# Kernel tuning notes

Hardware: AMD Instinct MI355X
Metric: run time of the kernel (lower is better)

Reference implementation:

```python
import jax, jax.numpy as jnp
import numpy as np


def _rotate_half(x):
    a, b = jnp.split(x, 2, axis=-1)
    return jnp.concatenate([-b, a], axis=-1)


def _rope_tables(L, d, dtype):
    inv = 1.0 / (10000.0 ** (jnp.arange(0, d, 2, dtype=jnp.float32) / d))
    ang = jnp.arange(L, dtype=jnp.float32)[:, None] * inv[None, :]  # (L, d/2)
    cos = jnp.repeat(jnp.cos(ang), 2, axis=-1)[None, :, None, :].astype(dtype)  # (1,L,1,d)
    sin = jnp.repeat(jnp.sin(ang), 2, axis=-1)[None, :, None, :].astype(dtype)
    return cos, sin


def setup_inputs() -> dict:
    key = jax.random.key(0)
    ks = jax.random.split(key, 7)
    B, L, D, h = 1, 1024, 768, 12
    d = D // h
    s = 0.02
    return {
        "X": jax.random.normal(ks[0], (B, L, D), jnp.float32),
        "Wq": jax.random.normal(ks[1], (D, D), jnp.float32) * s,
        "Wk": jax.random.normal(ks[2], (D, D), jnp.float32) * s,
        "Wv": jax.random.normal(ks[3], (D, D), jnp.float32) * s,
        "Wu": jax.random.normal(ks[4], (D, D), jnp.float32) * s,
        "Wg": jax.random.normal(ks[5], (3 * h, D), jnp.float32) * s,
        "Wo": jax.random.normal(ks[6], (D, D), jnp.float32) * s,
        "prior_mu": jnp.zeros((1, 1, h, d), jnp.float32),
        "prior_log_tau": jnp.zeros((1, 1, h, 1), jnp.float32),
    }


def _forward(X, Wq, Wk, Wv, Wu, Wg, Wo, prior_mu, prior_log_tau):
    B, L, D = X.shape
    h = prior_mu.shape[2]
    d = D // h
    eps = 1e-12
    # projections (torch Linear: x @ W.T, no bias)
    q = (X @ Wq.T).reshape(B, L, h, d)
    k = (X @ Wk.T).reshape(B, L, h, d)
    v = (X @ Wv.T).reshape(B, L, h, d)
    u = (X @ Wu.T).reshape(B, L, h, d)
    gate = (X @ Wg.T).reshape(B, L, h, 3)
    t = jnp.arange(1, L + 1, dtype=X.dtype).reshape(1, L, 1, 1)
    # calculate_logit (logit_type='deviation', causal)
    log_tau = jnp.exp(jnp.clip(prior_log_tau, -50.0, 30.0))
    u_sum = jnp.cumsum(u, axis=1)
    bar_u = (log_tau * prior_mu + u_sum) / (log_tau + t)
    s_i = -jnp.sum(u * bar_u, axis=-1, keepdims=True) / np.float32(np.sqrt(d))  # (B,L,h,1)
    # RoPE + L2 normalize q, k
    cos, sin = _rope_tables(L, d, X.dtype)
    q = q * cos + _rotate_half(q) * sin
    k = k * cos + _rotate_half(k) * sin
    q = q / jnp.maximum(jnp.linalg.norm(q, axis=-1, keepdims=True), eps)
    k = k / jnp.maximum(jnp.linalg.norm(k, axis=-1, keepdims=True), eps)
    # associative causal branch of compute_o
    s_max = jax.lax.stop_gradient(jnp.max(s_i, axis=1, keepdims=True))
    exp_s = jnp.exp(s_i - s_max)              # (B,L,h,1)
    E_t = jnp.cumsum(exp_s, axis=1)
    P_t = jnp.cumsum(s_i, axis=1)
    kv = jnp.einsum('blhd,blhe->blhde', k, v)  # (B,L,h,d,d)
    F_t = jnp.cumsum(exp_s[..., None] * kv, axis=1)
    G_t = jnp.cumsum(s_i[..., None] * kv, axis=1)
    H_t = jnp.cumsum(kv, axis=1)
    sig1 = jax.nn.sigmoid(gate[..., 0:1])      # (B,L,h,1)
    sigh = jax.nn.sigmoid(gate[..., 1:2])
    alpha = sigh / (E_t + eps)
    beta = (sig1 - sigh) / t
    gamma = -((beta * P_t + sigh) / t)
    M = alpha[..., None] * F_t + beta[..., None] * G_t + gamma[..., None] * H_t
    out = jnp.einsum('blhd,blhde->blhe', q, M)  # (B,L,h,d)
    # LayerNorm over head dim, eps=1e-5, no affine
    mu = jnp.mean(out, axis=-1, keepdims=True)
    var = jnp.mean(jnp.square(out - mu), axis=-1, keepdims=True)
    out = (out - mu) / jnp.sqrt(var + 1e-5)
    # output projection (dropout=0.0 -> identity)
    return out.reshape(B, L, D) @ Wo.T


def reference(X, Wq, Wk, Wv, Wu, Wg, Wo, prior_mu, prior_log_tau):
    return _forward(X, Wq, Wk, Wv, Wu, Wg, Wo, prior_mu, prior_log_tau)
```

## Files before the change

### kernel.cpp

```cpp
#include <hip/hip_runtime.h>
#include <hip/hip_bf16.h>
#include <math.h>

typedef __attribute__((ext_vector_type(8))) short bf16x8;
typedef __attribute__((ext_vector_type(4))) float f32x4;

#define SEQ 1024
#define DIM 768
#define NH 12
#define HD 64


__device__ __forceinline__ float wave_reduce_sum(float v) {
    for (int off = 1; off < 64; off <<= 1) v += __shfl_xor(v, off);
    return v;
}
__device__ __forceinline__ short f2bs(float x) {
    __hip_bfloat16 h = __float2bfloat16(x);
    return *reinterpret_cast<short*>(&h);
}
__device__ __forceinline__ float bs2f(short x) {
    __hip_bfloat16 h = *reinterpret_cast<__hip_bfloat16*>(&x);
    return (float)h;
}
__device__ __forceinline__ bf16x8 cvt8r(const float4& a, const float4& b) {
    bf16x8 r;
    r[0]=f2bs(a.x); r[1]=f2bs(a.y); r[2]=f2bs(a.z); r[3]=f2bs(a.w);
    r[4]=f2bs(b.x); r[5]=f2bs(b.y); r[6]=f2bs(b.z); r[7]=f2bs(b.w);
    return r;
}

__device__ __forceinline__ void async_copy16(const void* gptr, void* ldsbase, int lane) {
#if __has_builtin(__builtin_amdgcn_global_load_lds)
    __builtin_amdgcn_global_load_lds(
        (const __attribute__((address_space(1))) unsigned int*)gptr,
        (__attribute__((address_space(3))) unsigned int*)ldsbase, 16, 0, 0);
#else
    *(bf16x8*)((short*)ldsbase + lane*8) = *(const bf16x8*)gptr;
#endif
}

__global__ __launch_bounds__(256) void k_prep(const float* __restrict__ X,
    const float* __restrict__ Wq, const float* __restrict__ Wk,
    const float* __restrict__ Wv, const float* __restrict__ Wu,
    const float* __restrict__ Wg, const float* __restrict__ Wo,
    short* __restrict__ Xb, short* __restrict__ Wqb, short* __restrict__ Wkb,
    short* __restrict__ Wvb, short* __restrict__ Wub, short* __restrict__ Wgb,
    short* __restrict__ Wob)
{
    int seg = blockIdx.y;
    const float* src; short* dst; int n8;
    switch (seg) {
        case 0: src = X;  dst = Xb;  n8 = 98304; break;
        case 1: src = Wq; dst = Wqb; n8 = 73728; break;
        case 2: src = Wk; dst = Wkb; n8 = 73728; break;
        case 3: src = Wv; dst = Wvb; n8 = 73728; break;
        case 4: src = Wu; dst = Wub; n8 = 73728; break;
        case 5: src = Wg; dst = Wgb; n8 = 3456;  break;
        default: src = Wo; dst = Wob; n8 = 73728; break;
    }
    int i = blockIdx.x*256 + threadIdx.x;
    if (i >= n8) return;
    const float* s = src + (size_t)i*8;
    *(bf16x8*)(dst + (size_t)i*8) = cvt8r(*(const float4*)s, *(const float4*)(s + 4));
}

__global__ __launch_bounds__(256, 3) void k_proj5(const short* __restrict__ Xb,
    const short* __restrict__ Wqb, const short* __restrict__ Wkb,
    const short* __restrict__ Wvb, const short* __restrict__ Wub,
    const short* __restrict__ Wgb,
    __hip_bfloat16* __restrict__ Qb, __hip_bfloat16* __restrict__ Kb,
    __hip_bfloat16* __restrict__ Vt, __hip_bfloat16* __restrict__ Ub,
    float* __restrict__ G)
{
    int rt = blockIdx.x, ct = blockIdx.y, mat = blockIdx.z;
    if (mat == 4 && ct != 0) return;
    if (mat == 2 && rt >= 12) return;
    if ((mat == 0 || mat == 1 || mat == 3) && ct >= 6) return;

    __shared__ short lds[24576];

    int tid = threadIdx.x;
    int wv = tid>>6, lane = tid&63, g = lane>>4, n = lane&15;
    int wn = wv;

    const short* Asrc; const short* Bsrc; int arow0, brow0, Brows;
    if (mat == 2) { Asrc = Wvb; Bsrc = Xb; arow0 = rt*64; brow0 = ct*128; Brows = SEQ; }
    else {
        Asrc = Xb; arow0 = rt*64; brow0 = ct*128;
        Bsrc = (mat==0)?Wqb:(mat==1)?Wkb:(mat==3)?Wub:Wgb;
        Brows = (mat==4) ? 36 : DIM;
    }

    auto dma_step = [&](int buf, int k0) {
        short* Ab = lds + buf*4096;
        short* Bb = lds + 8192 + buf*8192;
        for (int p = 0; p < 2; ++p) {
            int sbase = p*256 + wv*64;
            int s = sbase + lane;
            int r = s >> 3, c = s & 7, cl = c ^ (r & 7);
            const short* gp = Asrc + (size_t)(arow0 + r)*DIM + k0 + cl*8;
            async_copy16(gp, Ab + sbase*8, lane);
        }
        for (int p = 0; p < 4; ++p) {
            int sbase = p*256 + wv*64;
            int s = sbase + lane;
            int r = s >> 3, c = s & 7, cl = c ^ (r & 7);
            int gr = brow0 + r; if (gr >= Brows) gr = Brows - 1;
            const short* gp = Bsrc + (size_t)gr*DIM + k0 + cl*8;
            async_copy16(gp, Bb + sbase*8, lane);
        }
    };

    f32x4 acc[4][2];
    for (int i=0;i<4;++i) for (int j=0;j<2;++j) acc[i][j] = (f32x4){0,0,0,0};

    dma_step(0, 0);
    for (int it = 0; it < 12; ++it) {
        __syncthreads();
        if (it < 11) dma_step(1 - (it & 1), (it + 1)*64);
        int buf = it & 1;
        const short* Ab = lds + buf*4096;
        const short* Bb = lds + 8192 + buf*8192;
        for (int ks = 0; ks < 2; ++ks) {
            int q = ks*4 + g;
            bf16x8 af[4], bfr[2];
            for (int i=0;i<4;++i)
                af[i] = *(const bf16x8*)(&Ab[((i*16+n)*8 + (q ^ (n&7)))*8]);
            for (int j=0;j<2;++j)
                bfr[j] = *(const bf16x8*)(&Bb[((wn*32+j*16+n)*8 + (q ^ (n&7)))*8]);
            for (int i=0;i<4;++i)
                for (int j=0;j<2;++j)
                    acc[i][j] = __builtin_amdgcn_mfma_f32_16x16x32_bf16(af[i], bfr[j], acc[i][j], 0,0,0);
        }
    }
    __syncthreads();

    if (mat == 4) {
        for (int i=0;i<4;++i) for (int j=0;j<2;++j) for (int r=0;r<4;++r) {
            int row = rt*64 + i*16 + g*4 + r;
            int col = wn*32 + j*16 + n;
            if (col < 36) G[(size_t)row*36 + col] = acc[i][j][r];
        }
        return;
    }

    short* C = lds;
    for (int i=0;i<4;++i) for (int j=0;j<2;++j) for (int r=0;r<4;++r)
        C[(i*16 + g*4 + r)*128 + wn*32 + j*16 + n] = f2bs(acc[i][j][r]);
    __syncthreads();

    if (mat == 2) {
        for (int k = 0; k < 16; ++k) {
            int row = k*4 + wv;
            unsigned int v = ((const unsigned int*)C)[row*64 + lane];
            ((unsigned int*)(Vt + (size_t)(rt*64 + row)*SEQ + ct*128))[lane] = v;
        }
    } else if (mat == 3) {
        for (int k = 0; k < 32; ++k) {
            int u = k*4 + wv;
            int row = u >> 1, hsel = u & 1;
            Ub[((size_t)(2*ct + hsel)*SEQ + rt*64 + row)*HD + lane] =
                *(__hip_bfloat16*)&C[row*128 + hsel*64 + lane];
        }
    } else {
        __hip_bfloat16* dst = (mat==0) ? Qb : Kb;
        int i2 = lane >> 1;
        float inv = expf((float)i2 * (-9.210340371976184f / 32.f));
        for (int k = 0; k < 32; ++k) {
            int u = k*4 + wv;
            int row = u >> 1, hsel = u & 1;
            int l = rt*64 + row;
            float x = bs2f(C[row*128 + hsel*64 + lane]);
            float ang = (float)l * inv;
            float c = cosf(ang), s = sinf(ang);
            float p = __shfl(x, lane ^ 32);
            float rot = (lane < 32) ? -p : p;
            float y = x*c + rot*s;
            float nrm = wave_reduce_sum(y*y);
            y = y / fmaxf(sqrtf(nrm), 1e-12f);
            dst[((size_t)(2*ct + hsel)*SEQ + l)*HD + lane] = __float2bfloat16(y);
        }
    }
}

__global__ __launch_bounds__(1024) void k_scan(const __hip_bfloat16* __restrict__ Ub,
    const float* __restrict__ G, const float* __restrict__ pmu,
    const float* __restrict__ plt,
    float* __restrict__ si_, float* __restrict__ es_, float* __restrict__ al_,
    float* __restrict__ be_, float* __restrict__ ga_)
{
    int h = blockIdx.x;
    int tid = threadIdx.x, wv = tid >> 6, lane = tid & 63;
    __shared__ float sbuf[SEQ], ebuf[SEQ], g1b[SEQ], ghb[SEQ];
    __shared__ float stot[16][64];
    __shared__ float wmax[16];
    __shared__ float smax_s;

    float ltv = fminf(fmaxf(plt[h], -50.f), 30.f);
    float ltau = expf(ltv);
    float mu = pmu[h*HD + lane];

    const __hip_bfloat16* up = Ub + ((size_t)h*SEQ + wv*64)*HD + lane;
    float Ul = 0.f;
    for (int i = 0; i < 64; ++i) Ul += (float)up[(size_t)i*HD];
    stot[wv][lane] = Ul;
    __syncthreads();
    float pre = ltau * mu;
    for (int w2 = 0; w2 < wv; ++w2) pre += stot[w2][lane];
    float V = pre;
    for (int i = 0; i < 64; ++i) {
        float uv = (float)up[(size_t)i*HD];
        V += uv;
        int l = wv*64 + i;
        float bar = V / (ltau + (float)(l + 1));
        float p = wave_reduce_sum(uv * bar);
        if (lane == 0) sbuf[l] = -p * 0.125f;
    }
    __syncthreads();
    float v = sbuf[tid];
    float vm = v;
    for (int off = 1; off < 64; off <<= 1) vm = fmaxf(vm, __shfl_xor(vm, off));
    if (lane == 0) wmax[wv] = vm;
    __syncthreads();
    if (wv == 0) {
        float mm = (lane < 16) ? wmax[lane] : -1e30f;
        for (int off = 1; off < 16; off <<= 1) mm = fmaxf(mm, __shfl_xor(mm, off));
        if (lane == 0) smax_s = mm;
    }
    __syncthreads();
    float ev = expf(fminf(v - smax_s, 0.f));
    ebuf[tid] = ev;
    g1b[tid] = 1.f / (1.f + expf(-G[(size_t)tid*36 + h*3 + 0]));
    ghb[tid] = 1.f / (1.f + expf(-G[(size_t)tid*36 + h*3 + 1]));
    si_[h*SEQ + tid] = v;
    es_[h*SEQ + tid] = ev;
    __syncthreads();
    if (wv == 0) {
        int base = lane * 16;
        float se = 0.f, ss = 0.f;
        for (int i = 0; i < 16; ++i) { se += ebuf[base + i]; ss += sbuf[base + i]; }
        float pe = se, ps = ss;
        for (int off = 1; off < 64; off <<= 1) {
            float t1 = __shfl_up(pe, off), t2 = __shfl_up(ps, off);
            if (lane >= off) { pe += t1; ps += t2; }
        }
        float E = pe - se, P = ps - ss;
        for (int i = 0; i < 16; ++i) {
            int l = base + i;
            E += ebuf[l]; P += sbuf[l];
            float t = (float)(l + 1);
            float s1 = g1b[l], sh = ghb[l];
            float a = sh / (E + 1e-12f);
            float b = (s1 - sh) / t;
            float gm = -((b * P + sh) / t);
            al_[h*SEQ + l] = a;
            be_[h*SEQ + l] = b;
            ga_[h*SEQ + l] = gm;
        }
    }
}

__global__ __launch_bounds__(256) void k_attn(const __hip_bfloat16* __restrict__ Qb,
    const __hip_bfloat16* __restrict__ Kb, const __hip_bfloat16* __restrict__ Vt,
    const float* __restrict__ si_, const float* __restrict__ es_,
    const float* __restrict__ al_, const float* __restrict__ be_,
    const float* __restrict__ ga_, __hip_bfloat16* __restrict__ opre)
{
    int t = blockIdx.x, h = blockIdx.y;
    int wv = threadIdx.x >> 6, lane = threadIdx.x & 63;
    int g = lane >> 4, n = lane & 15;
    __shared__ short P[4][16*64];
    __shared__ float Op[4][16][64];
    short* Pw = P[wv];
    int m0 = t*16;
    const short* qrow = (const short*)Qb + ((size_t)h*SEQ + m0 + n)*HD + g*8;
    bf16x8 qa0 = *(const bf16x8*)qrow;
    bf16x8 qa1 = *(const bf16x8*)(qrow + 32);
    const float* al = al_ + h*SEQ;
    const float* be = be_ + h*SEQ;
    const float* ga = ga_ + h*SEQ;
    const float* es = es_ + h*SEQ;
    const float* si = si_ + h*SEQ;
    float A_[4], B_[4], G_[4];
    for (int r = 0; r < 4; ++r) {
        int m = m0 + g*4 + r;
        A_[r] = al[m]; B_[r] = be[m]; G_[r] = ga[m];
    }
    f32x4 acco[4];
    for (int et = 0; et < 4; ++et) acco[et] = (f32x4){0.f,0.f,0.f,0.f};

    int jtmax = t >> 2;
    for (int jt = wv; jt <= jtmax; jt += 4) {
        int j0 = jt*64;
        for (int ct = 0; ct < 4; ++ct) {
            const short* krow = (const short*)Kb + ((size_t)h*SEQ + j0 + ct*16 + n)*HD + g*8;
            bf16x8 kb0 = *(const bf16x8*)krow;
            bf16x8 kb1 = *(const bf16x8*)(krow + 32);
            f32x4 sacc = {0.f,0.f,0.f,0.f};
            sacc = __builtin_amdgcn_mfma_f32_16x16x32_bf16(qa0, kb0, sacc, 0, 0, 0);
            sacc = __builtin_amdgcn_mfma_f32_16x16x32_bf16(qa1, kb1, sacc, 0, 0, 0);
            int j = j0 + ct*16 + n;
            float ej = es[j], sj = si[j];
            int chunk = ct*2 + (n>>3), e = n&7;
            for (int r = 0; r < 4; ++r) {
                int m = m0 + g*4 + r;
                float w = (j <= m) ? (A_[r]*ej + B_[r]*sj + G_[r]) : 0.f;
                int ml = g*4 + r;
                Pw[ml*64 + (chunk ^ (ml&7))*8 + e] = f2bs(w * sacc[r]);
            }
        }
        const short* vb = (const short*)Vt + (size_t)h*HD*SEQ;
        for (int et = 0; et < 4; ++et) {
            for (int sub = 0; sub < 2; ++sub) {
                int q = sub*4 + g;
                bf16x8 pa = *(const bf16x8*)(&Pw[n*64 + (q ^ (n&7))*8]);
                bf16x8 vfr = *(const bf16x8*)(vb + (size_t)(et*16 + n)*SEQ + j0 + sub*32 + g*8);
                acco[et] = __builtin_amdgcn_mfma_f32_16x16x32_bf16(pa, vfr, acco[et], 0, 0, 0);
            }
        }
    }
    for (int et = 0; et < 4; ++et)
        for (int r = 0; r < 4; ++r)
            Op[wv][g*4 + r][et*16 + n] = acco[et][r];
    __syncthreads();
    for (int rr = 0; rr < 4; ++rr) {
        int row = wv*4 + rr;
        float v = Op[0][row][lane] + Op[1][row][lane] + Op[2][row][lane] + Op[3][row][lane];
        float sm = wave_reduce_sum(v);
        float sq = wave_reduce_sum(v*v);
        float mu = sm * (1.f/64.f);
        float var = fmaxf(sq * (1.f/64.f) - mu*mu, 0.f);
        float invs = rsqrtf(var + 1e-5f);
        opre[(size_t)(m0 + row)*DIM + h*HD + lane] = __float2bfloat16((v - mu) * invs);
    }
}

__global__ __launch_bounds__(256, 4) void k_oproj(const short* __restrict__ A,
    const short* __restrict__ Wob, float* __restrict__ out)
{
    int rt = blockIdx.x, ct = blockIdx.y;
    __shared__ short lds[16384];

    int tid = threadIdx.x;
    int wv = tid>>6, lane = tid&63, g = lane>>4, n = lane&15;
    int wm = wv>>1, wn = wv&1;

    auto dma_step = [&](int buf, int k0) {
        short* Ab = lds + buf*4096;
        short* Bb = lds + 8192 + buf*4096;
        for (int p = 0; p < 2; ++p) {
            int sbase = p*256 + wv*64;
            int s = sbase + lane;
            int r = s >> 3, c = s & 7, cl = c ^ (r & 7);
            const short* ga_ = A + (size_t)(rt*64 + r)*DIM + k0 + cl*8;
            async_copy16(ga_, Ab + sbase*8, lane);
            const short* gb = Wob + (size_t)(ct*64 + r)*DIM + k0 + cl*8;
            async_copy16(gb, Bb + sbase*8, lane);
        }
    };

    f32x4 acc[2][2];
    for (int i=0;i<2;++i) for (int j=0;j<2;++j) acc[i][j] = (f32x4){0,0,0,0};

    dma_step(0, 0);
    for (int it = 0; it < 12; ++it) {
        __syncthreads();
        if (it < 11) dma_step(1 - (it & 1), (it + 1)*64);
        int buf = it & 1;
        const short* Ab = lds + buf*4096;
        const short* Bb = lds + 8192 + buf*4096;
        for (int ks = 0; ks < 2; ++ks) {
            int q = ks*4 + g;
            bf16x8 af[2], bfr[2];
            for (int i=0;i<2;++i)
                af[i] = *(const bf16x8*)(&Ab[((wm*32+i*16+n)*8 + (q ^ (n&7)))*8]);
            for (int j=0;j<2;++j)
                bfr[j] = *(const bf16x8*)(&Bb[((wn*32+j*16+n)*8 + (q ^ (n&7)))*8]);
            for (int i=0;i<2;++i)
                for (int j=0;j<2;++j)
                    acc[i][j] = __builtin_amdgcn_mfma_f32_16x16x32_bf16(af[i], bfr[j], acc[i][j], 0,0,0);
        }
    }
    for (int i=0;i<2;++i) for (int j=0;j<2;++j) for (int r=0;r<4;++r) {
        int row = rt*64 + wm*32 + i*16 + g*4 + r;
        int col = ct*64 + wn*32 + j*16 + n;
        out[(size_t)row*DIM + col] = acc[i][j][r];
    }
}

extern "C" void kernel_launch(void* const* d_in, const int* in_sizes, int n_in,
                              void* d_out, int out_size, void* d_ws, size_t ws_size,
                              hipStream_t stream) {
    const float* X   = (const float*)d_in[0];
    const float* Wq  = (const float*)d_in[1];
    const float* Wk  = (const float*)d_in[2];
    const float* Wv  = (const float*)d_in[3];
    const float* Wu  = (const float*)d_in[4];
    const float* Wg  = (const float*)d_in[5];
    const float* Wo  = (const float*)d_in[6];
    const float* pmu = (const float*)d_in[7];
    const float* plt = (const float*)d_in[8];

    char* w = (char*)d_ws;
    __hip_bfloat16* Qb   = (__hip_bfloat16*)(w + 0);
    __hip_bfloat16* Kb   = (__hip_bfloat16*)(w + 1572864);
    __hip_bfloat16* Vt   = (__hip_bfloat16*)(w + 3145728);
    __hip_bfloat16* opre = (__hip_bfloat16*)(w + 4718592);
    float*          G    = (float*)(w + 6291456);
    float*          si_  = (float*)(w + 6438912);
    float*          es_  = si_ + NH*SEQ;
    float*          al_  = es_ + NH*SEQ;
    float*          be_  = al_ + NH*SEQ;
    float*          ga_  = be_ + NH*SEQ;
    short*          Xb   = (short*)(w + 6684672);
    short*          Wqb  = (short*)(w + 8257536);
    short*          Wkb  = (short*)(w + 9437184);
    short*          Wvb  = (short*)(w + 10616832);
    short*          Wub  = (short*)(w + 11796480);
    short*          Wgb  = (short*)(w + 12976128);
    short*          Wob  = (short*)(w + 13031424);
    __hip_bfloat16* Ub   = (__hip_bfloat16*)d_out;
    float*          out  = (float*)d_out;

    hipLaunchKernelGGL(k_prep, dim3(384, 7), dim3(256), 0, stream,
                       X, Wq, Wk, Wv, Wu, Wg, Wo, Xb, Wqb, Wkb, Wvb, Wub, Wgb, Wob);
    hipLaunchKernelGGL(k_proj5, dim3(16, 8, 5), dim3(256), 0, stream,
                       Xb, Wqb, Wkb, Wvb, Wub, Wgb, Qb, Kb, Vt, Ub, G);
    hipLaunchKernelGGL(k_scan, dim3(NH), dim3(1024), 0, stream,
                       Ub, G, pmu, plt, si_, es_, al_, be_, ga_);
    hipLaunchKernelGGL(k_attn, dim3(64, NH), dim3(256), 0, stream,
                       Qb, Kb, Vt, si_, es_, al_, be_, ga_, opre);
    hipLaunchKernelGGL(k_oproj, dim3(16, 12), dim3(256), 0, stream,
                       (const short*)opre, Wob, out);
}
```

Measured before the change: 172.9 us.

## Fuse all five stages into one persistent cooperative kernel with grid syncs

Replaces the five separate kernel launches (convert, projections, scan, attention, output projection) with a single cooperative kernel of 400 blocks. The stages are separated by grid.sync calls, and each stage's work is assigned by block index. This removes the launch gaps and per-kernel ramp-up between stages. In exchange, every stage is limited to 400 blocks of 256 threads at occupancy 2, the scan stage appears to need a new partial-sum workspace, and each grid barrier has its own cost.

```diff
diff --git a/kernel.cpp b/kernel.cpp
--- a/kernel.cpp
+++ b/kernel.cpp
@@ -1,6 +1,9 @@
 #include <hip/hip_runtime.h>
 #include <hip/hip_bf16.h>
+#include <hip/hip_cooperative_groups.h>
 #include <math.h>
+
+namespace cg = cooperative_groups;
 
 typedef __attribute__((ext_vector_type(8))) short bf16x8;
 typedef __attribute__((ext_vector_type(4))) float f32x4;
@@ -9,10 +12,29 @@
 #define DIM 768
 #define NH 12
 #define HD 64
-
+#define NBLK 400
+
+#define OFF_QB   0
+#define OFF_KB   1572864
+#define OFF_VT   3145728
+#define OFF_OPRE 4718592
+#define OFF_G    6291456
+#define OFF_SCAL 6438912
+#define OFF_XB   6684672
+#define OFF_WQB  8257536
+#define OFF_WKB  9437184
+#define OFF_WVB  10616832
+#define OFF_WUB  11796480
+#define OFF_WGB  12976128
+#define OFF_WOB  13031424
+#define OFF_PSUM 14211072
 
 __device__ __forceinline__ float wave_reduce_sum(float v) {
     for (int off = 1; off < 64; off <<= 1) v += __shfl_xor(v, off);
+    return v;
+}
+__device__ __forceinline__ float wave_reduce_max(float v) {
+    for (int off = 1; off < 64; off <<= 1) v = fmaxf(v, __shfl_xor(v, off));
     return v;
 }
 __device__ __forceinline__ short f2bs(float x) {
@@ -29,7 +51,6 @@
     r[4]=f2bs(b.x); r[5]=f2bs(b.y); r[6]=f2bs(b.z); r[7]=f2bs(b.w);
     return r;
 }
-
 __device__ __forceinline__ void async_copy16(const void* gptr, void* ldsbase, int lane) {
 #if __has_builtin(__builtin_amdgcn_global_load_lds)
     __builtin_amdgcn_global_load_lds(
@@ -40,352 +61,364 @@
 #endif
 }
 
-__global__ __launch_bounds__(256) void k_prep(const float* __restrict__ X,
-    const float* __restrict__ Wq, const float* __restrict__ Wk,
-    const float* __restrict__ Wv, const float* __restrict__ Wu,
-    const float* __restrict__ Wg, const float* __restrict__ Wo,
-    short* __restrict__ Xb, short* __restrict__ Wqb, short* __restrict__ Wkb,
-    short* __restrict__ Wvb, short* __restrict__ Wub, short* __restrict__ Wgb,
-    short* __restrict__ Wob)
+__global__ __launch_bounds__(256, 2) void k_fused(
+    const float* __restrict__ X,  const float* __restrict__ Wq,
+    const float* __restrict__ Wk, const float* __restrict__ Wv,
+    const float* __restrict__ Wu, const float* __restrict__ Wg,
+    const float* __restrict__ Wo, const float* __restrict__ pmu,
+    const float* __restrict__ plt, char* __restrict__ ws, void* __restrict__ dout)
 {
-    int seg = blockIdx.y;
-    const float* src; short* dst; int n8;
-    switch (seg) {
-        case 0: src = X;  dst = Xb;  n8 = 98304; break;
-        case 1: src = Wq; dst = Wqb; n8 = 73728; break;
-        case 2: src = Wk; dst = Wkb; n8 = 73728; break;
-        case 3: src = Wv; dst = Wvb; n8 = 73728; break;
-        case 4: src = Wu; dst = Wub; n8 = 73728; break;
-        case 5: src = Wg; dst = Wgb; n8 = 3456;  break;
-        default: src = Wo; dst = Wob; n8 = 73728; break;
-    }
-    int i = blockIdx.x*256 + threadIdx.x;
-    if (i >= n8) return;
-    const float* s = src + (size_t)i*8;
-    *(bf16x8*)(dst + (size_t)i*8) = cvt8r(*(const float4*)s, *(const float4*)(s + 4));
-}
-
-__global__ __launch_bounds__(256, 3) void k_proj5(const short* __restrict__ Xb,
-    const short* __restrict__ Wqb, const short* __restrict__ Wkb,
-    const short* __restrict__ Wvb, const short* __restrict__ Wub,
-    const short* __restrict__ Wgb,
-    __hip_bfloat16* __restrict__ Qb, __hip_bfloat16* __restrict__ Kb,
-    __hip_bfloat16* __restrict__ Vt, __hip_bfloat16* __restrict__ Ub,
-    float* __restrict__ G)
-{
-    int rt = blockIdx.x, ct = blockIdx.y, mat = blockIdx.z;
-    if (mat == 4 && ct != 0) return;
-    if (mat == 2 && rt >= 12) return;
-    if ((mat == 0 || mat == 1 || mat == 3) && ct >= 6) return;
-
-    __shared__ short lds[24576];
-
-    int tid = threadIdx.x;
-    int wv = tid>>6, lane = tid&63, g = lane>>4, n = lane&15;
-    int wn = wv;
-
-    const short* Asrc; const short* Bsrc; int arow0, brow0, Brows;
-    if (mat == 2) { Asrc = Wvb; Bsrc = Xb; arow0 = rt*64; brow0 = ct*128; Brows = SEQ; }
-    else {
-        Asrc = Xb; arow0 = rt*64; brow0 = ct*128;
-        Bsrc = (mat==0)?Wqb:(mat==1)?Wkb:(mat==3)?Wub:Wgb;
-        Brows = (mat==4) ? 36 : DIM;
-    }
-
-    auto dma_step = [&](int buf, int k0) {
-        short* Ab = lds + buf*4096;
-        short* Bb = lds + 8192 + buf*8192;
-        for (int p = 0; p < 2; ++p) {
-            int sbase = p*256 + wv*64;
-            int s = sbase + lane;
-            int r = s >> 3, c = s & 7, cl = c ^ (r & 7);
-            const short* gp = Asrc + (size_t)(arow0 + r)*DIM + k0 + cl*8;
-            async_copy16(gp, Ab + sbase*8, lane);
-        }
-        for (int p = 0; p < 4; ++p) {
-            int sbase = p*256 + wv*64;
-            int s = sbase + lane;
-            int r = s >> 3, c = s & 7, cl = c ^ (r & 7);
-            int gr = brow0 + r; if (gr >= Brows) gr = Brows - 1;
-            const short* gp = Bsrc + (size_t)gr*DIM + k0 + cl*8;
-            async_copy16(gp, Bb + sbase*8, lane);
-        }
-    };
-
-    f32x4 acc[4][2];
-    for (int i=0;i<4;++i) for (int j=0;j<2;++j) acc[i][j] = (f32x4){0,0,0,0};
-
-    dma_step(0, 0);
-    for (int it = 0; it < 12; ++it) {
+    cg::grid_group grid = cg::this_grid();
+    alignas(16) __shared__ char smem[49152];
+
+    int bid = blockIdx.x, tid = threadIdx.x;
+    int wv = tid >> 6, lane = tid & 63, g = lane >> 4, n = lane & 15;
+
+    __hip_bfloat16* Qb   = (__hip_bfloat16*)(ws + OFF_QB);
+    __hip_bfloat16* Kb   = (__hip_bfloat16*)(ws + OFF_KB);
+    __hip_bfloat16* Vt   = (__hip_bfloat16*)(ws + OFF_VT);
+    __hip_bfloat16* opre = (__hip_bfloat16*)(ws + OFF_OPRE);
+    float* Gt  = (float*)(ws + OFF_G);
+    float* si_ = (float*)(ws + OFF_SCAL);
+    float* es_ = si_ + NH*SEQ;
+    float* al_ = es_ + NH*SEQ;
+    float* be_ = al_ + NH*SEQ;
+    float* ga_ = be_ + NH*SEQ;
+    short* Xb  = (short*)(ws + OFF_XB);
+    short* Wqb = (short*)(ws + OFF_WQB);
+    short* Wkb = (short*)(ws + OFF_WKB);
+    short* Wvb = (short*)(ws + OFF_WVB);
+    short* Wub = (short*)(ws + OFF_WUB);
+    short* Wgb = (short*)(ws + OFF_WGB);
+    short* Wob = (short*)(ws + OFF_WOB);
+    float* Psum = (float*)(ws + OFF_PSUM);
+    __hip_bfloat16* Ub = (__hip_bfloat16*)dout;
+    float* out = (float*)dout;
+
+    for (int idx = bid*256 + tid; idx < 470400; idx += NBLK*256) {
+        const float* src; short* dst; int off;
+        if      (idx < 98304)  { src = X;  dst = Xb;  off = idx; }
+        else if (idx < 172032) { src = Wq; dst = Wqb; off = idx - 98304; }
+        else if (idx < 245760) { src = Wk; dst = Wkb; off = idx - 172032; }
+        else if (idx < 319488) { src = Wv; dst = Wvb; off = idx - 245760; }
+        else if (idx < 393216) { src = Wu; dst = Wub; off = idx - 319488; }
+        else if (idx < 396672) { src = Wg; dst = Wgb; off = idx - 393216; }
+        else                   { src = Wo; dst = Wob; off = idx - 396672; }
+        const float* s = src + (size_t)off*8;
+        *(bf16x8*)(dst + (size_t)off*8) = cvt8r(*(const float4*)s, *(const float4*)(s + 4));
+    }
+    grid.sync();
+
+    {
+        int t = bid;
+        int mat, rt, ct;
+        if (t < 288)      { int m3 = t/96; mat = (m3==2)?3:m3; int r = t%96; rt = r/6; ct = r%6; }
+        else if (t < 384) { mat = 2; int r = t-288; rt = r/8; ct = r%8; }
+        else              { mat = 4; rt = t-384; ct = 0; }
+
+        short* lds = (short*)smem;
+        int wn = wv;
+
+        const short* Asrc; const short* Bsrc; int arow0, brow0, Brows;
+        if (mat == 2) { Asrc = Wvb; Bsrc = Xb; arow0 = rt*64; brow0 = ct*128; Brows = SEQ; }
+        else {
+            Asrc = Xb; arow0 = rt*64; brow0 = ct*128;
+            Bsrc = (mat==0)?Wqb:(mat==1)?Wkb:(mat==3)?Wub:Wgb;
+            Brows = (mat==4) ? 36 : DIM;
+        }
+
+        auto dma_step = [&](int buf, int k0) {
+            short* Ab = lds + buf*4096;
+            short* Bb = lds + 8192 + buf*8192;
+            for (int p = 0; p < 2; ++p) {
+                int sbase = p*256 + wv*64;
+                int s = sbase + lane;
+                int r = s >> 3, c = s & 7, cl = c ^ (r & 7);
+                async_copy16(Asrc + (size_t)(arow0 + r)*DIM + k0 + cl*8, Ab + sbase*8, lane);
+            }
+            for (int p = 0; p < 4; ++p) {
+                int sbase = p*256 + wv*64;
+                int s = sbase + lane;
+                int r = s >> 3, c = s & 7, cl = c ^ (r & 7);
+                int gr = brow0 + r; if (gr >= Brows) gr = Brows - 1;
+                async_copy16(Bsrc + (size_t)gr*DIM + k0 + cl*8, Bb + sbase*8, lane);
+            }
+        };
+
+        f32x4 acc[4][2];
+        for (int i=0;i<4;++i) for (int j=0;j<2;++j) acc[i][j] = (f32x4){0,0,0,0};
+
+        dma_step(0, 0);
+        for (int it = 0; it < 12; ++it) {
+            __syncthreads();
+            if (it < 11) dma_step(1 - (it & 1), (it + 1)*64);
+            int buf = it & 1;
+            const short* Ab = lds + buf*4096;
+            const short* Bb = lds + 8192 + buf*8192;
+            for (int ks = 0; ks < 2; ++ks) {
+                int q = ks*4 + g;
+                bf16x8 af[4], bfr[2];
+                for (int i=0;i<4;++i)
+                    af[i] = *(const bf16x8*)(&Ab[((i*16+n)*8 + (q ^ (n&7)))*8]);
+                for (int j=0;j<2;++j)
+                    bfr[j] = *(const bf16x8*)(&Bb[((wn*32+j*16+n)*8 + (q ^ (n&7)))*8]);
+                for (int i=0;i<4;++i)
+                    for (int j=0;j<2;++j)
+                        acc[i][j] = __builtin_amdgcn_mfma_f32_16x16x32_bf16(af[i], bfr[j], acc[i][j], 0,0,0);
+            }
+        }
         __syncthreads();
-        if (it < 11) dma_step(1 - (it & 1), (it + 1)*64);
-        int buf = it & 1;
-        const short* Ab = lds + buf*4096;
-        const short* Bb = lds + 8192 + buf*8192;
-        for (int ks = 0; ks < 2; ++ks) {
-            int q = ks*4 + g;
-            bf16x8 af[4], bfr[2];
-            for (int i=0;i<4;++i)
-                af[i] = *(const bf16x8*)(&Ab[((i*16+n)*8 + (q ^ (n&7)))*8]);
-            for (int j=0;j<2;++j)
-                bfr[j] = *(const bf16x8*)(&Bb[((wn*32+j*16+n)*8 + (q ^ (n&7)))*8]);
-            for (int i=0;i<4;++i)
-                for (int j=0;j<2;++j)
-                    acc[i][j] = __builtin_amdgcn_mfma_f32_16x16x32_bf16(af[i], bfr[j], acc[i][j], 0,0,0);
-        }
-    }
-    __syncthreads();
-
-    if (mat == 4) {
-        for (int i=0;i<4;++i) for (int j=0;j<2;++j) for (int r=0;r<4;++r) {
-            int row = rt*64 + i*16 + g*4 + r;
-            int col = wn*32 + j*16 + n;
-            if (col < 36) G[(size_t)row*36 + col] = acc[i][j][r];
-        }
-        return;
-    }
-
-    short* C = lds;
-    for (int i=0;i<4;++i) for (int j=0;j<2;++j) for (int r=0;r<4;++r)
-        C[(i*16 + g*4 + r)*128 + wn*32 + j*16 + n] = f2bs(acc[i][j][r]);
-    __syncthreads();
-
-    if (mat == 2) {
-        for (int k = 0; k < 16; ++k) {
-            int row = k*4 + wv;
-            unsigned int v = ((const unsigned int*)C)[row*64 + lane];
-            ((unsigned int*)(Vt + (size_t)(rt*64 + row)*SEQ + ct*128))[lane] = v;
-        }
-    } else if (mat == 3) {
-        for (int k = 0; k < 32; ++k) {
-            int u = k*4 + wv;
-            int row = u >> 1, hsel = u & 1;
-            Ub[((size_t)(2*ct + hsel)*SEQ + rt*64 + row)*HD + lane] =
-                *(__hip_bfloat16*)&C[row*128 + hsel*64 + lane];
-        }
-    } else {
-        __hip_bfloat16* dst = (mat==0) ? Qb : Kb;
-        int i2 = lane >> 1;
-        float inv = expf((float)i2 * (-9.210340371976184f / 32.f));
-        for (int k = 0; k < 32; ++k) {
-            int u = k*4 + wv;
-            int row = u >> 1, hsel = u & 1;
-            int l = rt*64 + row;
-            float x = bs2f(C[row*128 + hsel*64 + lane]);
-            float ang = (float)l * inv;
-            float c = cosf(ang), s = sinf(ang);
-            float p = __shfl(x, lane ^ 32);
-            float rot = (lane < 32) ? -p : p;
-            float y = x*c + rot*s;
-            float nrm = wave_reduce_sum(y*y);
-            y = y / fmaxf(sqrtf(nrm), 1e-12f);
-            dst[((size_t)(2*ct + hsel)*SEQ + l)*HD + lane] = __float2bfloat16(y);
-        }
-    }
-}
-
-__global__ __launch_bounds__(1024) void k_scan(const __hip_bfloat16* __restrict__ Ub,
-    const float* __restrict__ G, const float* __restrict__ pmu,
-    const float* __restrict__ plt,
-    float* __restrict__ si_, float* __restrict__ es_, float* __restrict__ al_,
-    float* __restrict__ be_, float* __restrict__ ga_)
-{
-    int h = blockIdx.x;
-    int tid = threadIdx.x, wv = tid >> 6, lane = tid & 63;
-    __shared__ float sbuf[SEQ], ebuf[SEQ], g1b[SEQ], ghb[SEQ];
-    __shared__ float stot[16][64];
-    __shared__ float wmax[16];
-    __shared__ float smax_s;
-
-    float ltv = fminf(fmaxf(plt[h], -50.f), 30.f);
-    float ltau = expf(ltv);
-    float mu = pmu[h*HD + lane];
-
-    const __hip_bfloat16* up = Ub + ((size_t)h*SEQ + wv*64)*HD + lane;
-    float Ul = 0.f;
-    for (int i = 0; i < 64; ++i) Ul += (float)up[(size_t)i*HD];
-    stot[wv][lane] = Ul;
-    __syncthreads();
-    float pre = ltau * mu;
-    for (int w2 = 0; w2 < wv; ++w2) pre += stot[w2][lane];
-    float V = pre;
-    for (int i = 0; i < 64; ++i) {
-        float uv = (float)up[(size_t)i*HD];
-        V += uv;
-        int l = wv*64 + i;
-        float bar = V / (ltau + (float)(l + 1));
-        float p = wave_reduce_sum(uv * bar);
-        if (lane == 0) sbuf[l] = -p * 0.125f;
-    }
-    __syncthreads();
-    float v = sbuf[tid];
-    float vm = v;
-    for (int off = 1; off < 64; off <<= 1) vm = fmaxf(vm, __shfl_xor(vm, off));
-    if (lane == 0) wmax[wv] = vm;
-    __syncthreads();
-    if (wv == 0) {
-        float mm = (lane < 16) ? wmax[lane] : -1e30f;
-        for (int off = 1; off < 16; off <<= 1) mm = fmaxf(mm, __shfl_xor(mm, off));
-        if (lane == 0) smax_s = mm;
-    }
-    __syncthreads();
-    float ev = expf(fminf(v - smax_s, 0.f));
-    ebuf[tid] = ev;
-    g1b[tid] = 1.f / (1.f + expf(-G[(size_t)tid*36 + h*3 + 0]));
-    ghb[tid] = 1.f / (1.f + expf(-G[(size_t)tid*36 + h*3 + 1]));
-    si_[h*SEQ + tid] = v;
-    es_[h*SEQ + tid] = ev;
-    __syncthreads();
-    if (wv == 0) {
-        int base = lane * 16;
-        float se = 0.f, ss = 0.f;
-        for (int i = 0; i < 16; ++i) { se += ebuf[base + i]; ss += sbuf[base + i]; }
-        float pe = se, ps = ss;
-        for (int off = 1; off < 64; off <<= 1) {
-            float t1 = __shfl_up(pe, off), t2 = __shfl_up(ps, off);
-            if (lane >= off) { pe += t1; ps += t2; }
-        }
-        float E = pe - se, P = ps - ss;
-        for (int i = 0; i < 16; ++i) {
-            int l = base + i;
-            E += ebuf[l]; P += sbuf[l];
-            float t = (float)(l + 1);
-            float s1 = g1b[l], sh = ghb[l];
-            float a = sh / (E + 1e-12f);
-            float b = (s1 - sh) / t;
-            float gm = -((b * P + sh) / t);
-            al_[h*SEQ + l] = a;
-            be_[h*SEQ + l] = b;
-            ga_[h*SEQ + l] = gm;
-        }
-    }
-}
-
-__global__ __launch_bounds__(256) void k_attn(const __hip_bfloat16* __restrict__ Qb,
-    const __hip_bfloat16* __restrict__ Kb, const __hip_bfloat16* __restrict__ Vt,
-    const float* __restrict__ si_, const float* __restrict__ es_,
-    const float* __restrict__ al_, const float* __restrict__ be_,
-    const float* __restrict__ ga_, __hip_bfloat16* __restrict__ opre)
-{
-    int t = blockIdx.x, h = blockIdx.y;
-    int wv = threadIdx.x >> 6, lane = threadIdx.x & 63;
-    int g = lane >> 4, n = lane & 15;
-    __shared__ short P[4][16*64];
-    __shared__ float Op[4][16][64];
-    short* Pw = P[wv];
-    int m0 = t*16;
-    const short* qrow = (const short*)Qb + ((size_t)h*SEQ + m0 + n)*HD + g*8;
-    bf16x8 qa0 = *(const bf16x8*)qrow;
-    bf16x8 qa1 = *(const bf16x8*)(qrow + 32);
-    const float* al = al_ + h*SEQ;
-    const float* be = be_ + h*SEQ;
-    const float* ga = ga_ + h*SEQ;
-    const float* es = es_ + h*SEQ;
-    const float* si = si_ + h*SEQ;
-    float A_[4], B_[4], G_[4];
-    for (int r = 0; r < 4; ++r) {
-        int m = m0 + g*4 + r;
-        A_[r] = al[m]; B_[r] = be[m]; G_[r] = ga[m];
-    }
-    f32x4 acco[4];
-    for (int et = 0; et < 4; ++et) acco[et] = (f32x4){0.f,0.f,0.f,0.f};
-
-    int jtmax = t >> 2;
-    for (int jt = wv; jt <= jtmax; jt += 4) {
-        int j0 = jt*64;
-        for (int ct = 0; ct < 4; ++ct) {
-            const short* krow = (const short*)Kb + ((size_t)h*SEQ + j0 + ct*16 + n)*HD + g*8;
-            bf16x8 kb0 = *(const bf16x8*)krow;
-            bf16x8 kb1 = *(const bf16x8*)(krow + 32);
-            f32x4 sacc = {0.f,0.f,0.f,0.f};
-            sacc = __builtin_amdgcn_mfma_f32_16x16x32_bf16(qa0, kb0, sacc, 0, 0, 0);
-            sacc = __builtin_amdgcn_mfma_f32_16x16x32_bf16(qa1, kb1, sacc, 0, 0, 0);
-            int j = j0 + ct*16 + n;
-            float ej = es[j], sj = si[j];
-            int chunk = ct*2 + (n>>3), e = n&7;
+
+        if (mat == 4) {
+            for (int i=0;i<4;++i) for (int j=0;j<2;++j) for (int r=0;r<4;++r) {
+                int row = rt*64 + i*16 + g*4 + r;
+                int col = wn*32 + j*16 + n;
+                if (col < 36) Gt[(size_t)row*36 + col] = acc[i][j][r];
+            }
+        } else {
+            short* C = lds;
+            for (int i=0;i<4;++i) for (int j=0;j<2;++j) for (int r=0;r<4;++r)
+                C[(i*16 + g*4 + r)*128 + wn*32 + j*16 + n] = f2bs(acc[i][j][r]);
+            __syncthreads();
+
+            if (mat == 2) {
+                for (int k = 0; k < 16; ++k) {
+                    int row = k*4 + wv;
+                    unsigned int v = ((const unsigned int*)C)[row*64 + lane];
+                    ((unsigned int*)(Vt + (size_t)(rt*64 + row)*SEQ + ct*128))[lane] = v;
+                }
+            } else if (mat == 3) {
+                for (int k = 0; k < 32; ++k) {
+                    int u = k*4 + wv;
+                    int row = u >> 1, hsel = u & 1;
+                    Ub[((size_t)(2*ct + hsel)*SEQ + rt*64 + row)*HD + lane] =
+                        *(__hip_bfloat16*)&C[row*128 + hsel*64 + lane];
+                }
+            } else {
+                __hip_bfloat16* dst = (mat==0) ? Qb : Kb;
+                int i2 = lane >> 1;
+                float inv = expf((float)i2 * (-9.210340371976184f / 32.f));
+                for (int k = 0; k < 32; ++k) {
+                    int u = k*4 + wv;
+                    int row = u >> 1, hsel = u & 1;
+                    int l = rt*64 + row;
+                    float x = bs2f(C[row*128 + hsel*64 + lane]);
+                    float ang = (float)l * inv;
+                    float c = cosf(ang), s = sinf(ang);
+                    float p = __shfl(x, lane ^ 32);
+                    float rot = (lane < 32) ? -p : p;
+                    float y = x*c + rot*s;
+                    float nrm = wave_reduce_sum(y*y);
+                    y = y / fmaxf(sqrtf(nrm), 1e-12f);
+                    dst[((size_t)(2*ct + hsel)*SEQ + l)*HD + lane] = __float2bfloat16(y);
+                }
+            }
+        }
+    }
+    grid.sync();
+
+    if (bid < 48) {
+        int t = bid*4 + wv;
+        int h = t >> 4, chunk = t & 15;
+        const __hip_bfloat16* up = Ub + ((size_t)h*SEQ + chunk*64)*HD + lane;
+        float s = 0.f;
+        for (int i = 0; i < 64; ++i) s += (float)up[(size_t)i*HD];
+        Psum[((size_t)h*16 + chunk)*64 + lane] = s;
+    }
+    grid.sync();
+
+    if (bid < 48) {
+        int t = bid*4 + wv;
+        int h = t >> 4, chunk = t & 15;
+        float ltv = fminf(fmaxf(plt[h], -50.f), 30.f);
+        float ltau = expf(ltv);
+        float mu = pmu[h*HD + lane];
+        float V = ltau * mu;
+        for (int c = 0; c < chunk; ++c) V += Psum[((size_t)h*16 + c)*64 + lane];
+        const __hip_bfloat16* up = Ub + ((size_t)h*SEQ + chunk*64)*HD + lane;
+        for (int i = 0; i < 64; ++i) {
+            float uv = (float)up[(size_t)i*HD];
+            V += uv;
+            int l = chunk*64 + i;
+            float bar = V / (ltau + (float)(l + 1));
+            float p = wave_reduce_sum(uv * bar);
+            if (lane == 0) si_[h*SEQ + l] = -p * 0.125f;
+        }
+    }
+    grid.sync();
+
+    if (bid < NH) {
+        int h = bid;
+        float* sb = (float*)smem;
+        float* eb = sb + 1024;
+        float* g1 = eb + 1024;
+        float* gh = g1 + 1024;
+        float* redu = gh + 1024;
+        float vmax = -1e30f;
+        for (int r = 0; r < 4; ++r) {
+            int l = r*256 + tid;
+            float v = si_[h*SEQ + l];
+            sb[l] = v;
+            vmax = fmaxf(vmax, v);
+        }
+        vmax = wave_reduce_max(vmax);
+        if (lane == 0) redu[wv] = vmax;
+        __syncthreads();
+        float smax = fmaxf(fmaxf(redu[0], redu[1]), fmaxf(redu[2], redu[3]));
+        for (int r = 0; r < 4; ++r) {
+            int l = r*256 + tid;
+            float ev = expf(fminf(sb[l] - smax, 0.f));
+            eb[l] = ev;
+            es_[h*SEQ + l] = ev;
+            g1[l] = 1.f / (1.f + expf(-Gt[(size_t)l*36 + h*3 + 0]));
+            gh[l] = 1.f / (1.f + expf(-Gt[(size_t)l*36 + h*3 + 1]));
+        }
+        __syncthreads();
+        if (wv == 0) {
+            int base = lane * 16;
+            float se = 0.f, ss = 0.f;
+            for (int i = 0; i < 16; ++i) { se += eb[base + i]; ss += sb[base + i]; }
+            float pe = se, ps = ss;
+            for (int off = 1; off < 64; off <<= 1) {
+                float t1 = __shfl_up(pe, off), t2 = __shfl_up(ps, off);
+                if (lane >= off) { pe += t1; ps += t2; }
+            }
+            float E = pe - se, P = ps - ss;
+            for (int i = 0; i < 16; ++i) {
+                int l = base + i;
+                E += eb[l]; P += sb[l];
+                float t = (float)(l + 1);
+                float s1 = g1[l], sh = gh[l];
+                float a = sh / (E + 1e-12f);
+                float b = (s1 - sh) / t;
+                float gm = -((b * P + sh) / t);
+                al_[h*SEQ + l] = a;
+                be_[h*SEQ + l] = b;
+                ga_[h*SEQ + l] = gm;
+            }
+        }
+    }
+    grid.sync();
+
+    for (int rep = 0; rep < 2; ++rep) {
+        int task = bid + rep*NBLK;
+        if (task < 768) {
+            int t = task & 63, h = task >> 6;
+            short* P  = (short*)smem;
+            float* Op = (float*)(smem + 8192);
+            short* Pw = P + wv*1024;
+            int m0 = t*16;
+            const short* qrow = (const short*)Qb + ((size_t)h*SEQ + m0 + n)*HD + g*8;
+            bf16x8 qa0 = *(const bf16x8*)qrow;
+            bf16x8 qa1 = *(const bf16x8*)(qrow + 32);
+            const float* al = al_ + h*SEQ;
+            const float* be = be_ + h*SEQ;
+            const float* ga = ga_ + h*SEQ;
+            const float* es = es_ + h*SEQ;
+            const float* si = si_ + h*SEQ;
+            float A_[4], B_[4], G_[4];
             for (int r = 0; r < 4; ++r) {
                 int m = m0 + g*4 + r;
-                float w = (j <= m) ? (A_[r]*ej + B_[r]*sj + G_[r]) : 0.f;
-                int ml = g*4 + r;
-                Pw[ml*64 + (chunk ^ (ml&7))*8 + e] = f2bs(w * sacc[r]);
-            }
-        }
-        const short* vb = (const short*)Vt + (size_t)h*HD*SEQ;
-        for (int et = 0; et < 4; ++et) {
-            for (int sub = 0; sub < 2; ++sub) {
-                int q = sub*4 + g;
-                bf16x8 pa = *(const bf16x8*)(&Pw[n*64 + (q ^ (n&7))*8]);
-                bf16x8 vfr = *(const bf16x8*)(vb + (size_t)(et*16 + n)*SEQ + j0 + sub*32 + g*8);
-                acco[et] = __builtin_amdgcn_mfma_f32_16x16x32_bf16(pa, vfr, acco[et], 0, 0, 0);
-            }
-        }
-    }
-    for (int et = 0; et < 4; ++et)
-        for (int r = 0; r < 4; ++r)
-            Op[wv][g*4 + r][et*16 + n] = acco[et][r];
-    __syncthreads();
-    for (int rr = 0; rr < 4; ++rr) {
-        int row = wv*4 + rr;
-        float v = Op[0][row][lane] + Op[1][row][lane] + Op[2][row][lane] + Op[3][row][lane];
-        float sm = wave_reduce_sum(v);
-        float sq = wave_reduce_sum(v*v);
-        float mu = sm * (1.f/64.f);
-        float var = fmaxf(sq * (1.f/64.f) - mu*mu, 0.f);
-        float invs = rsqrtf(var + 1e-5f);
-        opre[(size_t)(m0 + row)*DIM + h*HD + lane] = __float2bfloat16((v - mu) * invs);
-    }
-}
-
-__global__ __launch_bounds__(256, 4) void k_oproj(const short* __restrict__ A,
-    const short* __restrict__ Wob, float* __restrict__ out)
-{
-    int rt = blockIdx.x, ct = blockIdx.y;
-    __shared__ short lds[16384];
-
-    int tid = threadIdx.x;
-    int wv = tid>>6, lane = tid&63, g = lane>>4, n = lane&15;
-    int wm = wv>>1, wn = wv&1;
-
-    auto dma_step = [&](int buf, int k0) {
-        short* Ab = lds + buf*4096;
-        short* Bb = lds + 8192 + buf*4096;
-        for (int p = 0; p < 2; ++p) {
-            int sbase = p*256 + wv*64;
-            int s = sbase + lane;
-            int r = s >> 3, c = s & 7, cl = c ^ (r & 7);
-            const short* ga_ = A + (size_t)(rt*64 + r)*DIM + k0 + cl*8;
-            async_copy16(ga_, Ab + sbase*8, lane);
-            const short* gb = Wob + (size_t)(ct*64 + r)*DIM + k0 + cl*8;
-            async_copy16(gb, Bb + sbase*8, lane);
-        }
-    };
-
-    f32x4 acc[2][2];
-    for (int i=0;i<2;++i) for (int j=0;j<2;++j) acc[i][j] = (f32x4){0,0,0,0};
-
-    dma_step(0, 0);
-    for (int it = 0; it < 12; ++it) {
-        __syncthreads();
-        if (it < 11) dma_step(1 - (it & 1), (it + 1)*64);
-        int buf = it & 1;
-        const short* Ab = lds + buf*4096;
-        const short* Bb = lds + 8192 + buf*4096;
-        for (int ks = 0; ks < 2; ++ks) {
-            int q = ks*4 + g;
-            bf16x8 af[2], bfr[2];
-            for (int i=0;i<2;++i)
-                af[i] = *(const bf16x8*)(&Ab[((wm*32+i*16+n)*8 + (q ^ (n&7)))*8]);
-            for (int j=0;j<2;++j)
-                bfr[j] = *(const bf16x8*)(&Bb[((wn*32+j*16+n)*8 + (q ^ (n&7)))*8]);
-            for (int i=0;i<2;++i)
+                A_[r] = al[m]; B_[r] = be[m]; G_[r] = ga[m];
+            }
+            f32x4 acco[4];
+            for (int et = 0; et < 4; ++et) acco[et] = (f32x4){0.f,0.f,0.f,0.f};
+
+            int jtmax = t >> 2;
+            for (int jt = wv; jt <= jtmax; jt += 4) {
+                int j0 = jt*64;
+                for (int ct = 0; ct < 4; ++ct) {
+                    const short* krow = (const short*)Kb + ((size_t)h*SEQ + j0 + ct*16 + n)*HD + g*8;
+                    bf16x8 kb0 = *(const bf16x8*)krow;
+                    bf16x8 kb1 = *(const bf16x8*)(krow + 32);
+                    f32x4 sacc = {0.f,0.f,0.f,0.f};
+                    sacc = __builtin_amdgcn_mfma_f32_16x16x32_bf16(qa0, kb0, sacc, 0, 0, 0);
+                    sacc = __builtin_amdgcn_mfma_f32_16x16x32_bf16(qa1, kb1, sacc, 0, 0, 0);
+                    int j = j0 + ct*16 + n;
+                    float ej = es[j], sj = si[j];
+                    int chunk = ct*2 + (n>>3), e = n&7;
+                    for (int r = 0; r < 4; ++r) {
+                        int m = m0 + g*4 + r;
+                        float w = (j <= m) ? (A_[r]*ej + B_[r]*sj + G_[r]) : 0.f;
+                        int ml = g*4 + r;
+                        Pw[ml*64 + (chunk ^ (ml&7))*8 + e] = f2bs(w * sacc[r]);
+                    }
+                }
+                const short* vb = (const short*)Vt + (size_t)h*HD*SEQ;
+                for (int et = 0; et < 4; ++et) {
+                    for (int sub = 0; sub < 2; ++sub) {
+                        int q = sub*4 + g;
+                        bf16x8 pa = *(const bf16x8*)(&Pw[n*64 + (q ^ (n&7))*8]);
+                        bf16x8 vfr = *(const bf16x8*)(vb + (size_t)(et*16 + n)*SEQ + j0 + sub*32 + g*8);
+                        acco[et] = __builtin_amdgcn_mfma_f32_16x16x32_bf16(pa, vfr, acco[et], 0, 0, 0);
+                    }
+                }
+            }
+            for (int et = 0; et < 4; ++et)
+                for (int r = 0; r < 4; ++r)
+                    Op[(wv*16 + g*4 + r)*64 + et*16 + n] = acco[et][r];
+            __syncthreads();
+            for (int rr = 0; rr < 4; ++rr) {
+                int row = wv*4 + rr;
+                float v = Op[row*64 + lane] + Op[(16 + row)*64 + lane]
+                        + Op[(32 + row)*64 + lane] + Op[(48 + row)*64 + lane];
+                float sm = wave_reduce_sum(v);
+                float sq = wave_reduce_sum(v*v);
+                float mu = sm * (1.f/64.f);
+                float var = fmaxf(sq * (1.f/64.f) - mu*mu, 0.f);
+                float invs = rsqrtf(var + 1e-5f);
+                opre[(size_t)(m0 + row)*DIM + h*HD + lane] = __float2bfloat16((v - mu) * invs);
+            }
+            __syncthreads();
+        }
+    }
+    grid.sync();
+
+    if (bid < 192) {
+        int rt = bid / 12, ct = bid % 12;
+        short* lds = (short*)smem;
+        int wm = wv>>1, wn = wv&1;
+        const short* A = (const short*)opre;
+
+        auto dma_step = [&](int buf, int k0) {
+            short* Ab = lds + buf*4096;
+            short* Bb = lds + 8192 + buf*4096;
+            for (int p = 0; p < 2; ++p) {
+                int sbase = p*256 + wv*64;
+                int s = sbase + lane;
+                int r = s >> 3, c = s & 7, cl = c ^ (r & 7);
+                async_copy16(A + (size_t)(rt*64 + r)*DIM + k0 + cl*8, Ab + sbase*8, lane);
+                async_copy16(Wob + (size_t)(ct*64 + r)*DIM + k0 + cl*8, Bb + sbase*8, lane);
+            }
+        };
+
+        f32x4 acc[2][2];
+        for (int i=0;i<2;++i) for (int j=0;j<2;++j) acc[i][j] = (f32x4){0,0,0,0};
+
+        dma_step(0, 0);
+        for (int it = 0; it < 12; ++it) {
+            __syncthreads();
+            if (it < 11) dma_step(1 - (it & 1), (it + 1)*64);
+            int buf = it & 1;
+            const short* Ab = lds + buf*4096;
+            const short* Bb = lds + 8192 + buf*4096;
+            for (int ks = 0; ks < 2; ++ks) {
+                int q = ks*4 + g;
+                bf16x8 af[2], bfr[2];
+                for (int i=0;i<2;++i)
+                    af[i] = *(const bf16x8*)(&Ab[((wm*32+i*16+n)*8 + (q ^ (n&7)))*8]);
                 for (int j=0;j<2;++j)
-                    acc[i][j] = __builtin_amdgcn_mfma_f32_16x16x32_bf16(af[i], bfr[j], acc[i][j], 0,0,0);
-        }
-    }
-    for (int i=0;i<2;++i) for (int j=0;j<2;++j) for (int r=0;r<4;++r) {
-        int row = rt*64 + wm*32 + i*16 + g*4 + r;
-        int col = ct*64 + wn*32 + j*16 + n;
-        out[(size_t)row*DIM + col] = acc[i][j][r];
+                    bfr[j] = *(const bf16x8*)(&Bb[((wn*32+j*16+n)*8 + (q ^ (n&7)))*8]);
+                for (int i=0;i<2;++i)
+                    for (int j=0;j<2;++j)
+                        acc[i][j] = __builtin_amdgcn_mfma_f32_16x16x32_bf16(af[i], bfr[j], acc[i][j], 0,0,0);
+            }
+        }
+        for (int i=0;i<2;++i) for (int j=0;j<2;++j) for (int r=0;r<4;++r) {
+            int row = rt*64 + wm*32 + i*16 + g*4 + r;
+            int col = ct*64 + wn*32 + j*16 + n;
+            out[(size_t)row*DIM + col] = acc[i][j][r];
+        }
     }
 }
 
@@ -401,36 +434,12 @@
     const float* Wo  = (const float*)d_in[6];
     const float* pmu = (const float*)d_in[7];
     const float* plt = (const float*)d_in[8];
-
-    char* w = (char*)d_ws;
-    __hip_bfloat16* Qb   = (__hip_bfloat16*)(w + 0);
-    __hip_bfloat16* Kb   = (__hip_bfloat16*)(w + 1572864);
-    __hip_bfloat16* Vt   = (__hip_bfloat16*)(w + 3145728);
-    __hip_bfloat16* opre = (__hip_bfloat16*)(w + 4718592);
-    float*          G    = (float*)(w + 6291456);
-    float*          si_  = (float*)(w + 6438912);
-    float*          es_  = si_ + NH*SEQ;
-    float*          al_  = es_ + NH*SEQ;
-    float*          be_  = al_ + NH*SEQ;
-    float*          ga_  = be_ + NH*SEQ;
-    short*          Xb   = (short*)(w + 6684672);
-    short*          Wqb  = (short*)(w + 8257536);
-    short*          Wkb  = (short*)(w + 9437184);
-    short*          Wvb  = (short*)(w + 10616832);
-    short*          Wub  = (short*)(w + 11796480);
-    short*          Wgb  = (short*)(w + 12976128);
-    short*          Wob  = (short*)(w + 13031424);
-    __hip_bfloat16* Ub   = (__hip_bfloat16*)d_out;
-    float*          out  = (float*)d_out;
-
-    hipLaunchKernelGGL(k_prep, dim3(384, 7), dim3(256), 0, stream,
-                       X, Wq, Wk, Wv, Wu, Wg, Wo, Xb, Wqb, Wkb, Wvb, Wub, Wgb, Wob);
-    hipLaunchKernelGGL(k_proj5, dim3(16, 8, 5), dim3(256), 0, stream,
-                       Xb, Wqb, Wkb, Wvb, Wub, Wgb, Qb, Kb, Vt, Ub, G);
-    hipLaunchKernelGGL(k_scan, dim3(NH), dim3(1024), 0, stream,
-                       Ub, G, pmu, plt, si_, es_, al_, be_, ga_);
-    hipLaunchKernelGGL(k_attn, dim3(64, NH), dim3(256), 0, stream,
-                       Qb, Kb, Vt, si_, es_, al_, be_, ga_, opre);
-    hipLaunchKernelGGL(k_oproj, dim3(16, 12), dim3(256), 0, stream,
-                       (const short*)opre, Wob, out);
-}
+    char* ws = (char*)d_ws;
+    void* dout = d_out;
+
+    void* args[] = { (void*)&X, (void*)&Wq, (void*)&Wk, (void*)&Wv, (void*)&Wu,
+                     (void*)&Wg, (void*)&Wo, (void*)&pmu, (void*)&plt,
+                     (void*)&ws, (void*)&dout };
+    hipLaunchCooperativeKernel((const void*)k_fused, dim3(NBLK), dim3(256),
+                               args, 0, stream);
+}
```

Result: slower. 453.4 us (+162.3%).
